# Kernel tuning notes

Measured on AMD Instinct MI355X. Metric: run time of the kernel, lower is better.

Reference implementation:

```python
import jax, jax.numpy as jnp
import numpy as np

K = 5
PAD = K // 2
EPS = 1e-12  # F.normalize eps


def setup_inputs() -> dict:
    key = jax.random.key(0)
    k1, k2, k3 = jax.random.split(key, 3)
    b, c, h, w = 8, 1024, 64, 64
    out_ch = 1024
    feature = jax.random.normal(k1, (b, c, h, w), dtype=jnp.float32)
    # Conv2d(1024 + K*K, out_ch, 1) -> weight [out_ch, 1049], bias [out_ch]
    conv_w = jax.random.normal(k2, (out_ch, c + K * K), dtype=jnp.float32) * 0.02
    conv_b = jax.random.normal(k3, (out_ch,), dtype=jnp.float32) * 0.02
    return {"feature": feature, "conv_w": conv_w, "conv_b": conv_b}


def reference(feature, conv_w, conv_b):
    b, c, h, w = feature.shape
    # L2-normalize over channel dim (F.normalize: x / max(||x||, eps))
    norm = jnp.sqrt(jnp.sum(feature * feature, axis=1, keepdims=True))
    fn = feature / jnp.maximum(norm, EPS)
    fp = jnp.pad(fn, ((0, 0), (0, 0), (PAD, PAD), (PAD, PAD)))
    # 25 shifted correlations; order matches torch loop: index = col*K + row
    corr = jnp.stack(
        [jnp.sum(fp[:, :, r:h + r, cc:w + cc] * fn, axis=1)
         for cc in range(K) for r in range(K)],
        axis=1,
    )  # [b, K*K, h, w]
    cat = jnp.concatenate([feature, corr], axis=1)  # [b, c+K*K, h, w]
    y = jnp.einsum('oc,bchw->bohw', conv_w, cat) + conv_b[None, :, None, None]
    return jax.nn.relu(y)
```

## Files before the change

### kernel.cpp

```cpp
#include <hip/hip_runtime.h>
#include <hip/hip_bf16.h>


typedef __attribute__((ext_vector_type(8))) short short8x;
typedef __attribute__((ext_vector_type(4))) float floatx4;

#define B_   8
#define C_   1024
#define HW_  4096
#define KPAD 1088
#define NT   17

__device__ __forceinline__ unsigned short f2bf(float f) {
  unsigned int u = __float_as_uint(f);
  u += 0x7FFFu + ((u >> 16) & 1u);
  return (unsigned short)(u >> 16);
}
__device__ __forceinline__ float bf2f(unsigned short s) {
  return __uint_as_float(((unsigned int)s) << 16);
}

__device__ __forceinline__ void async16(const void* g, void* l) {
  __builtin_amdgcn_global_load_lds(
      (__attribute__((address_space(1))) void*)(void*)g,
      (__attribute__((address_space(3))) void*)l, 16, 0, 0);
}

__device__ __forceinline__ short8x rd16(const char* p) {
  return *(const short8x*)p;
}

__global__ __launch_bounds__(512) void scn_corr_part(
    const float* __restrict__ f, float* __restrict__ part) {
  const int tid = threadIdx.x;
  const int x = tid & 63;
  const int y = blockIdx.x * 8 + (tid >> 6);
  const int cs = blockIdx.y, b = blockIdx.z;

  const int xs0 = (x + 2 < 64) ? x + 2 : 63;
  const int xs1 = (x + 1 < 64) ? x + 1 : 63;
  const int xs3 = (x - 1 >= 0) ? x - 1 : 0;
  const int xs4 = (x - 2 >= 0) ? x - 2 : 0;

  const bool ym2 = (y >= 2), ym1 = (y >= 1), yp1 = (y <= 62), yp2 = (y <= 61);

  const float* rp0 = f + ((size_t)b * C_ + cs * 128) * HW_ + y * 64;

  float h[25];
#pragma unroll
  for (int j = 0; j < 25; ++j) h[j] = 0.f;

#pragma unroll 4
  for (int c = 0; c < 128; ++c) {
    const float* rp = rp0 + (size_t)c * HW_;
    const float ctr = rp[x];
    const float vm2 = ym2 ? rp[x - 128] : 0.f;
    const float vm1 = ym1 ? rp[x - 64] : 0.f;
    const float vp1 = yp1 ? rp[x + 64] : 0.f;
    const float vp2 = yp2 ? rp[x + 128] : 0.f;
    const float c0 = rp[xs0], c1 = rp[xs1], c3 = rp[xs3], c4 = rp[xs4];
    const float v[5] = {vm2, vm1, ctr, vp1, vp2};
    const float cc[5] = {c0, c1, ctr, c3, c4};
#pragma unroll
    for (int dxi = 0; dxi < 5; ++dxi)
#pragma unroll
      for (int dyi = 0; dyi < 5; ++dyi)
        h[dxi * 5 + dyi] = fmaf(v[dyi], cc[dxi], h[dxi * 5 + dyi]);
  }

  float* pb = part + (size_t)(cs * 25) * 32768 + b * HW_ + y * 64;
#pragma unroll
  for (int j = 0; j < 25; ++j) {
    const int dx = (j / 5) - 2;
    const int tgt = x - dx;
    const int wx = (tgt + 64) & 63;
    const float val = ((unsigned)tgt < 64u) ? h[j] : 0.f;
    pb[(size_t)j * 32768 + wx] = val;
  }
}

__global__ __launch_bounds__(256) void scn_transpose(
    const float* __restrict__ f, unsigned short* __restrict__ At) {
  __shared__ float lds[64][65];
  const int mt = blockIdx.x, kt = blockIdx.y, b = blockIdx.z;
  const int tid = threadIdx.x;
  const float* src = f + ((size_t)b * C_ + kt * 64) * HW_ + mt * 64;
  const int mi = tid & 63, kr = tid >> 6;
#pragma unroll
  for (int i = 0; i < 16; ++i)
    lds[kr + i * 4][mi] = src[(size_t)(kr + i * 4) * HW_ + mi];
  __syncthreads();
  unsigned short* dst = At + ((size_t)b * HW_ + mt * 64) * KPAD + kt * 64;
  const int c = tid & 7, mr = tid >> 3;
#pragma unroll
  for (int half = 0; half < 2; ++half) {
    const int mm = mr + half * 32;
    short8x v;
#pragma unroll
    for (int j = 0; j < 8; ++j) v[j] = (short)f2bf(lds[c * 8 + j][mm]);
    *(short8x*)(dst + (size_t)mm * KPAD + c * 8) = v;
  }
}

__global__ __launch_bounds__(256) void scn_invn(const float* __restrict__ part,
                                                float* __restrict__ invn) {
  const int i = blockIdx.x * 256 + threadIdx.x;
  float s = 0.f;
#pragma unroll
  for (int cs = 0; cs < 8; ++cs) s += part[(size_t)(cs * 25 + 12) * 32768 + i];
  invn[i] = 1.0f / fmaxf(sqrtf(s), 1e-12f);
}

__global__ __launch_bounds__(256) void scn_corr_reduce(
    const float* __restrict__ part, const float* __restrict__ invn,
    unsigned short* __restrict__ At) {
  const int b = blockIdx.y;
  const int m = blockIdx.x * 256 + threadIdx.x;
  const int i = b * HW_ + m;
  const int y = m >> 6, x = m & 63;

  float acc[25];
#pragma unroll
  for (int j = 0; j < 25; ++j) acc[j] = 0.f;
#pragma unroll 1
  for (int cs = 0; cs < 8; ++cs) {
    const float* pb = part + (size_t)(cs * 25) * 32768 + i;
#pragma unroll
    for (int j = 0; j < 25; ++j) acc[j] += pb[(size_t)j * 32768];
  }
  const float ic = invn[i];
  unsigned short r[64];
#pragma unroll
  for (int j = 0; j < 25; ++j) {
    const int dy = (j % 5) - 2, dx = (j / 5) - 2;
    const int ny = y + dy, nx = x + dx;
    float in2 = (ny >= 0 && ny < 64 && nx >= 0 && nx < 64)
                    ? invn[b * HW_ + (ny << 6) + nx] : 0.f;
    r[j] = f2bf(acc[j] * ic * in2);
  }
#pragma unroll
  for (int j = 25; j < 64; ++j) r[j] = 0;
  unsigned short* row = At + ((size_t)b * HW_ + m) * KPAD + 1024;
#pragma unroll
  for (int v = 0; v < 8; ++v) *(short8x*)(row + v * 8) = *(short8x*)(r + v * 8);
}

__global__ __launch_bounds__(256) void scn_wcast(const float* __restrict__ w,
                                                 unsigned short* __restrict__ Wb) {
  const int i = blockIdx.x * 256 + threadIdx.x;
  const int o = i / KPAD, k = i - o * KPAD;
  Wb[i] = (k < 1049) ? f2bf(w[(size_t)o * 1049 + k]) : 0;
}

__global__ __launch_bounds__(512, 2) void scn_gemm(
    const unsigned short* __restrict__ Wb, const unsigned short* __restrict__ At,
    const float* __restrict__ bias, float* __restrict__ out) {
  extern __shared__ char lds[];
  const int tid = threadIdx.x;
  const int l = tid & 63;
  const int wid = tid >> 6;
  const int wm = wid >> 2;
  const int wn = wid & 3;
  const int nb = blockIdx.x, ob = blockIdx.y, b = blockIdx.z;

  const int rr = tid >> 3;
  const int cswz = ((tid & 7) ^ (rr & 7)) << 3;
  const unsigned short* gA = Wb + (size_t)(ob * 256 + rr) * KPAD + cswz;
  const unsigned short* gB = At + ((size_t)b * HW_ + nb * 256 + rr) * KPAD + cswz;
  char* const dBase = (char*)lds + tid * 16;

#define ISSUE_A(bf, kt)                                         \
  do {                                                          \
    const unsigned short* _s = gA + (kt) * 64;                  \
    char* _d = dBase + (bf) * 65536;                            \
    async16(_s, _d);                                            \
    async16(_s + (size_t)64 * KPAD, _d + 8192);                 \
    async16(_s + (size_t)128 * KPAD, _d + 16384);               \
    async16(_s + (size_t)192 * KPAD, _d + 24576);               \
  } while (0)

#define ISSUE_B(bf, kt)                                         \
  do {                                                          \
    const unsigned short* _s = gB + (kt) * 64;                  \
    char* _d = dBase + (bf) * 65536 + 32768;                    \
    async16(_s, _d);                                            \
    async16(_s + (size_t)64 * KPAD, _d + 8192);                 \
    async16(_s + (size_t)128 * KPAD, _d + 16384);               \
    async16(_s + (size_t)192 * KPAD, _d + 24576);               \
  } while (0)

  const int l15 = l & 15, l4g = l >> 4, l7 = l & 7;
  const int aoff0 = l15 * 128 + ((l4g ^ l7) << 4);
  const int aoff1 = l15 * 128 + (((l4g + 4) ^ l7) << 4);
  const char* aB0 = (const char*)lds + wm * 16384;
  const char* bB0 = (const char*)lds + 32768 + (wn >> 1) * 16384 + (wn & 1) * 8192;

  floatx4 acc[8][4];
#pragma unroll
  for (int i = 0; i < 8; ++i)
#pragma unroll
    for (int j = 0; j < 4; ++j) acc[i][j] = (floatx4){0.f, 0.f, 0.f, 0.f};

  ISSUE_A(0, 0); ISSUE_B(0, 0);
  ISSUE_A(1, 1); ISSUE_B(1, 1);
  asm volatile("s_waitcnt vmcnt(8)" ::: "memory");
  __builtin_amdgcn_s_barrier();

  short8x a[4][2], b0[2][2], b1[2][2];

  for (int t = 0; t < NT; ++t) {
    const int bf = t & 1;
    const char* ab = aB0 + bf * 65536;
    const char* bb = bB0 + bf * 65536;
    const int t2 = (t < NT - 2) ? (t + 2) : 0;

#pragma unroll
    for (int i = 0; i < 4; ++i) {
      a[i][0] = rd16(ab + i * 2048 + aoff0);
      a[i][1] = rd16(ab + i * 2048 + aoff1);
    }
#pragma unroll
    for (int j = 0; j < 2; ++j) {
      b0[j][0] = rd16(bb + j * 2048 + aoff0);
      b0[j][1] = rd16(bb + j * 2048 + aoff1);
    }
    __builtin_amdgcn_s_barrier();
    asm volatile("s_waitcnt lgkmcnt(0)" ::: "memory");
    __builtin_amdgcn_sched_barrier(0);
    __builtin_amdgcn_s_setprio(1);
#pragma unroll
    for (int i = 0; i < 4; ++i)
#pragma unroll
      for (int j = 0; j < 2; ++j) {
        acc[i][j] = __builtin_amdgcn_mfma_f32_16x16x32_bf16(a[i][0], b0[j][0], acc[i][j], 0, 0, 0);
        acc[i][j] = __builtin_amdgcn_mfma_f32_16x16x32_bf16(a[i][1], b0[j][1], acc[i][j], 0, 0, 0);
      }
    __builtin_amdgcn_s_setprio(0);
    __builtin_amdgcn_s_barrier();

#pragma unroll
    for (int j = 0; j < 2; ++j) {
      b1[j][0] = rd16(bb + (2 + j) * 2048 + aoff0);
      b1[j][1] = rd16(bb + (2 + j) * 2048 + aoff1);
    }
    __builtin_amdgcn_s_barrier();
    asm volatile("s_waitcnt lgkmcnt(0)" ::: "memory");
    __builtin_amdgcn_sched_barrier(0);
    __builtin_amdgcn_s_setprio(1);
#pragma unroll
    for (int i = 0; i < 4; ++i)
#pragma unroll
      for (int j = 0; j < 2; ++j) {
        acc[i][2 + j] = __builtin_amdgcn_mfma_f32_16x16x32_bf16(a[i][0], b1[j][0], acc[i][2 + j], 0, 0, 0);
        acc[i][2 + j] = __builtin_amdgcn_mfma_f32_16x16x32_bf16(a[i][1], b1[j][1], acc[i][2 + j], 0, 0, 0);
      }
    __builtin_amdgcn_s_setprio(0);
    __builtin_amdgcn_s_barrier();

#pragma unroll
    for (int i = 0; i < 4; ++i) {
      a[i][0] = rd16(ab + (4 + i) * 2048 + aoff0);
      a[i][1] = rd16(ab + (4 + i) * 2048 + aoff1);
    }
    ISSUE_B(bf, t2);
    __builtin_amdgcn_s_barrier();
    asm volatile("s_waitcnt lgkmcnt(0)" ::: "memory");
    __builtin_amdgcn_sched_barrier(0);
    __builtin_amdgcn_s_setprio(1);
#pragma unroll
    for (int i = 0; i < 4; ++i)
#pragma unroll
      for (int j = 0; j < 2; ++j) {
        acc[4 + i][2 + j] = __builtin_amdgcn_mfma_f32_16x16x32_bf16(a[i][0], b1[j][0], acc[4 + i][2 + j], 0, 0, 0);
        acc[4 + i][2 + j] = __builtin_amdgcn_mfma_f32_16x16x32_bf16(a[i][1], b1[j][1], acc[4 + i][2 + j], 0, 0, 0);
      }
    __builtin_amdgcn_s_setprio(0);
    __builtin_amdgcn_s_barrier();

    ISSUE_A(bf, t2);
    __builtin_amdgcn_s_barrier();
    __builtin_amdgcn_s_setprio(1);
#pragma unroll
    for (int i = 0; i < 4; ++i)
#pragma unroll
      for (int j = 0; j < 2; ++j) {
        acc[4 + i][j] = __builtin_amdgcn_mfma_f32_16x16x32_bf16(a[i][0], b0[j][0], acc[4 + i][j], 0, 0, 0);
        acc[4 + i][j] = __builtin_amdgcn_mfma_f32_16x16x32_bf16(a[i][1], b0[j][1], acc[4 + i][j], 0, 0, 0);
      }
    __builtin_amdgcn_s_setprio(0);
    asm volatile("s_waitcnt vmcnt(8)" ::: "memory");
    __builtin_amdgcn_s_barrier();
  }
  asm volatile("s_waitcnt vmcnt(0)" ::: "memory");
#undef ISSUE_A
#undef ISSUE_B

  float* outb = out + (size_t)b * C_ * HW_;
#pragma unroll
  for (int i = 0; i < 8; ++i) {
    const int o0 = ob * 256 + wm * 128 + i * 16 + l4g * 4;
    float bs[4];
#pragma unroll
    for (int r = 0; r < 4; ++r) bs[r] = bias[o0 + r];
#pragma unroll
    for (int j = 0; j < 4; ++j) {
      const int m = nb * 256 + wn * 64 + j * 16 + l15;
#pragma unroll
      for (int r = 0; r < 4; ++r) {
        float v = acc[i][j][r] + bs[r];
        outb[(size_t)(o0 + r) * HW_ + m] = v > 0.f ? v : 0.f;
      }
    }
  }
}

extern "C" void kernel_launch(void* const* d_in, const int* in_sizes, int n_in,
                              void* d_out, int out_size, void* d_ws, size_t ws_size,
                              hipStream_t stream) {
  const float* feature = (const float*)d_in[0];
  const float* conv_w  = (const float*)d_in[1];
  const float* conv_b  = (const float*)d_in[2];
  float* out = (float*)d_out;

  char* ws = (char*)d_ws;
  unsigned short* At = (unsigned short*)(ws);
  float* part        = (float*)(ws + 71303168);
  unsigned short* Wb = (unsigned short*)(ws + 71303168);
  float* invn        = (float*)(ws + 97517568);

  static int gemm_attr_set = 0;
  if (!gemm_attr_set) {
    hipFuncSetAttribute((const void*)scn_gemm,
                        hipFuncAttributeMaxDynamicSharedMemorySize, 131072);
    gemm_attr_set = 1;
  }

  scn_corr_part<<<dim3(8, 8, 8), 512, 0, stream>>>(feature, part);
  scn_transpose<<<dim3(64, 16, 8), 256, 0, stream>>>(feature, At);
  scn_invn<<<dim3(128), 256, 0, stream>>>(part, invn);
  scn_corr_reduce<<<dim3(16, 8), 256, 0, stream>>>(part, invn, At);
  scn_wcast<<<dim3((1024 * KPAD) / 256), 256, 0, stream>>>(conv_w, Wb);
  scn_gemm<<<dim3(16, 4, 8), 512, 131072, stream>>>(Wb, At, conv_b, out);
}
```

Measured before the change: 383.2 us.

## Fuse bf16 transpose of features into correlation partial kernel

The separate transpose kernel, which re-read the whole fp32 feature tensor to build the bf16 K-major GEMM operand, is removed. The correlation kernel now converts each centre value it already loads to bf16, stages a 512x64 tile in LDS, and writes the transposed rows to At after each 64-channel half. This saves one full read of the 128 MB input and one kernel launch. In exchange the correlation kernel gains about 66 KB of LDS, which can lower occupancy, plus two extra barriers per half.

```diff
diff --git a/kernel.cpp b/kernel.cpp
--- a/kernel.cpp
+++ b/kernel.cpp
@@ -16,9 +16,6 @@
   u += 0x7FFFu + ((u >> 16) & 1u);
   return (unsigned short)(u >> 16);
 }
-__device__ __forceinline__ float bf2f(unsigned short s) {
-  return __uint_as_float(((unsigned int)s) << 16);
-}
 
 __device__ __forceinline__ void async16(const void* g, void* l) {
   __builtin_amdgcn_global_load_lds(
@@ -31,7 +28,10 @@
 }
 
 __global__ __launch_bounds__(512) void scn_corr_part(
-    const float* __restrict__ f, float* __restrict__ part) {
+    const float* __restrict__ f, float* __restrict__ part,
+    unsigned short* __restrict__ At) {
+  __shared__ unsigned short lct[512][66];
+
   const int tid = threadIdx.x;
   const int x = tid & 63;
   const int y = blockIdx.x * 8 + (tid >> 6);
@@ -50,22 +50,43 @@
 #pragma unroll
   for (int j = 0; j < 25; ++j) h[j] = 0.f;
 
+  unsigned short* const lrow = &lct[tid][0];
+  const int m0 = blockIdx.x * 512;
+  const int cslice = tid & 7, mbase = tid >> 3;
+
+  for (int half = 0; half < 2; ++half) {
 #pragma unroll 4
-  for (int c = 0; c < 128; ++c) {
-    const float* rp = rp0 + (size_t)c * HW_;
-    const float ctr = rp[x];
-    const float vm2 = ym2 ? rp[x - 128] : 0.f;
-    const float vm1 = ym1 ? rp[x - 64] : 0.f;
-    const float vp1 = yp1 ? rp[x + 64] : 0.f;
-    const float vp2 = yp2 ? rp[x + 128] : 0.f;
-    const float c0 = rp[xs0], c1 = rp[xs1], c3 = rp[xs3], c4 = rp[xs4];
-    const float v[5] = {vm2, vm1, ctr, vp1, vp2};
-    const float cc[5] = {c0, c1, ctr, c3, c4};
-#pragma unroll
-    for (int dxi = 0; dxi < 5; ++dxi)
-#pragma unroll
-      for (int dyi = 0; dyi < 5; ++dyi)
-        h[dxi * 5 + dyi] = fmaf(v[dyi], cc[dxi], h[dxi * 5 + dyi]);
+    for (int c64 = 0; c64 < 64; ++c64) {
+      const int c = half * 64 + c64;
+      const float* rp = rp0 + (size_t)c * HW_;
+      const float ctr = rp[x];
+      const float vm2 = ym2 ? rp[x - 128] : 0.f;
+      const float vm1 = ym1 ? rp[x - 64] : 0.f;
+      const float vp1 = yp1 ? rp[x + 64] : 0.f;
+      const float vp2 = yp2 ? rp[x + 128] : 0.f;
+      const float c0 = rp[xs0], c1 = rp[xs1], c3 = rp[xs3], c4 = rp[xs4];
+      lrow[c64] = f2bf(ctr);
+      const float v[5] = {vm2, vm1, ctr, vp1, vp2};
+      const float cc[5] = {c0, c1, ctr, c3, c4};
+#pragma unroll
+      for (int dxi = 0; dxi < 5; ++dxi)
+#pragma unroll
+        for (int dyi = 0; dyi < 5; ++dyi)
+          h[dxi * 5 + dyi] = fmaf(v[dyi], cc[dxi], h[dxi * 5 + dyi]);
+    }
+    __syncthreads();
+    const int k0 = cs * 128 + half * 64;
+#pragma unroll
+    for (int g = 0; g < 8; ++g) {
+      const int mm = mbase + g * 64;
+      const unsigned int* p =
+          (const unsigned int*)((const char*)&lct[mm][0] + cslice * 16);
+      unsigned int w0 = p[0], w1 = p[1], w2 = p[2], w3 = p[3];
+      unsigned int* dst = (unsigned int*)(At + ((size_t)b * HW_ + m0 + mm) * KPAD +
+                                          k0 + cslice * 8);
+      dst[0] = w0; dst[1] = w1; dst[2] = w2; dst[3] = w3;
+    }
+    __syncthreads();
   }
 
   float* pb = part + (size_t)(cs * 25) * 32768 + b * HW_ + y * 64;
@@ -76,29 +97,6 @@
     const int wx = (tgt + 64) & 63;
     const float val = ((unsigned)tgt < 64u) ? h[j] : 0.f;
     pb[(size_t)j * 32768 + wx] = val;
-  }
-}
-
-__global__ __launch_bounds__(256) void scn_transpose(
-    const float* __restrict__ f, unsigned short* __restrict__ At) {
-  __shared__ float lds[64][65];
-  const int mt = blockIdx.x, kt = blockIdx.y, b = blockIdx.z;
-  const int tid = threadIdx.x;
-  const float* src = f + ((size_t)b * C_ + kt * 64) * HW_ + mt * 64;
-  const int mi = tid & 63, kr = tid >> 6;
-#pragma unroll
-  for (int i = 0; i < 16; ++i)
-    lds[kr + i * 4][mi] = src[(size_t)(kr + i * 4) * HW_ + mi];
-  __syncthreads();
-  unsigned short* dst = At + ((size_t)b * HW_ + mt * 64) * KPAD + kt * 64;
-  const int c = tid & 7, mr = tid >> 3;
-#pragma unroll
-  for (int half = 0; half < 2; ++half) {
-    const int mm = mr + half * 32;
-    short8x v;
-#pragma unroll
-    for (int j = 0; j < 8; ++j) v[j] = (short)f2bf(lds[c * 8 + j][mm]);
-    *(short8x*)(dst + (size_t)mm * KPAD + c * 8) = v;
   }
 }
 
@@ -335,8 +333,7 @@
     gemm_attr_set = 1;
   }
 
-  scn_corr_part<<<dim3(8, 8, 8), 512, 0, stream>>>(feature, part);
-  scn_transpose<<<dim3(64, 16, 8), 256, 0, stream>>>(feature, At);
+  scn_corr_part<<<dim3(8, 8, 8), 512, 0, stream>>>(feature, part, At);
   scn_invn<<<dim3(128), 256, 0, stream>>>(part, invn);
   scn_corr_reduce<<<dim3(16, 8), 256, 0, stream>>>(part, invn, At);
   scn_wcast<<<dim3((1024 * KPAD) / 256), 256, 0, stream>>>(conv_w, Wb);
```

Measured after the change: 460.3 us. 1.2x slower.

## Fuse correlation-partial and transpose kernels into one interleaved launch, use shuffles

Applied to the files above, without the earlier changes.

Merges the shifted-correlation partial-sum kernel and the bf16 transpose kernel into a single launch of 4608 blocks. Every ninth block runs correlation work and the other eight each transpose two 64x64 tiles, so the long-running correlation blocks overlap with memory-bound transposes and one launch is removed. Horizontal neighbor loads in the correlation loop are replaced with wave shuffles of the center value. The cost is that correlation blocks now reserve the larger LDS footprint they never use, which can lower occupancy for them.

```diff
diff --git a/kernel.cpp b/kernel.cpp
--- a/kernel.cpp
+++ b/kernel.cpp
@@ -16,9 +16,6 @@
   u += 0x7FFFu + ((u >> 16) & 1u);
   return (unsigned short)(u >> 16);
 }
-__device__ __forceinline__ float bf2f(unsigned short s) {
-  return __uint_as_float(((unsigned int)s) << 16);
-}
 
 __device__ __forceinline__ void async16(const void* g, void* l) {
   __builtin_amdgcn_global_load_lds(
@@ -30,75 +27,84 @@
   return *(const short8x*)p;
 }
 
-__global__ __launch_bounds__(512) void scn_corr_part(
-    const float* __restrict__ f, float* __restrict__ part) {
+__global__ __launch_bounds__(512) void scn_aux(
+    const float* __restrict__ f, float* __restrict__ part,
+    unsigned short* __restrict__ At) {
+  __shared__ float lds2[2][64][65];
+  const int n = blockIdx.x;
+  const int g = n / 9, r = n - g * 9;
   const int tid = threadIdx.x;
-  const int x = tid & 63;
-  const int y = blockIdx.x * 8 + (tid >> 6);
-  const int cs = blockIdx.y, b = blockIdx.z;
-
-  const int xs0 = (x + 2 < 64) ? x + 2 : 63;
-  const int xs1 = (x + 1 < 64) ? x + 1 : 63;
-  const int xs3 = (x - 1 >= 0) ? x - 1 : 0;
-  const int xs4 = (x - 2 >= 0) ? x - 2 : 0;
-
-  const bool ym2 = (y >= 2), ym1 = (y >= 1), yp1 = (y <= 62), yp2 = (y <= 61);
-
-  const float* rp0 = f + ((size_t)b * C_ + cs * 128) * HW_ + y * 64;
-
-  float h[25];
-#pragma unroll
-  for (int j = 0; j < 25; ++j) h[j] = 0.f;
+
+  if (r == 0) {
+    const int x = tid & 63;
+    const int y = (g & 7) * 8 + (tid >> 6);
+    const int cs = (g >> 3) & 7, b = g >> 6;
+
+    const int xs0 = (x + 2 < 64) ? x + 2 : 63;
+    const int xs1 = (x + 1 < 64) ? x + 1 : 63;
+    const int xs3 = (x - 1 >= 0) ? x - 1 : 0;
+    const int xs4 = (x - 2 >= 0) ? x - 2 : 0;
+
+    const bool ym2 = (y >= 2), ym1 = (y >= 1), yp1 = (y <= 62), yp2 = (y <= 61);
+
+    const float* rp0 = f + ((size_t)b * C_ + cs * 128) * HW_ + y * 64;
+
+    float h[25];
+#pragma unroll
+    for (int j = 0; j < 25; ++j) h[j] = 0.f;
 
 #pragma unroll 4
-  for (int c = 0; c < 128; ++c) {
-    const float* rp = rp0 + (size_t)c * HW_;
-    const float ctr = rp[x];
-    const float vm2 = ym2 ? rp[x - 128] : 0.f;
-    const float vm1 = ym1 ? rp[x - 64] : 0.f;
-    const float vp1 = yp1 ? rp[x + 64] : 0.f;
-    const float vp2 = yp2 ? rp[x + 128] : 0.f;
-    const float c0 = rp[xs0], c1 = rp[xs1], c3 = rp[xs3], c4 = rp[xs4];
-    const float v[5] = {vm2, vm1, ctr, vp1, vp2};
-    const float cc[5] = {c0, c1, ctr, c3, c4};
-#pragma unroll
-    for (int dxi = 0; dxi < 5; ++dxi)
-#pragma unroll
-      for (int dyi = 0; dyi < 5; ++dyi)
-        h[dxi * 5 + dyi] = fmaf(v[dyi], cc[dxi], h[dxi * 5 + dyi]);
-  }
-
-  float* pb = part + (size_t)(cs * 25) * 32768 + b * HW_ + y * 64;
-#pragma unroll
-  for (int j = 0; j < 25; ++j) {
-    const int dx = (j / 5) - 2;
-    const int tgt = x - dx;
-    const int wx = (tgt + 64) & 63;
-    const float val = ((unsigned)tgt < 64u) ? h[j] : 0.f;
-    pb[(size_t)j * 32768 + wx] = val;
-  }
-}
-
-__global__ __launch_bounds__(256) void scn_transpose(
-    const float* __restrict__ f, unsigned short* __restrict__ At) {
-  __shared__ float lds[64][65];
-  const int mt = blockIdx.x, kt = blockIdx.y, b = blockIdx.z;
-  const int tid = threadIdx.x;
-  const float* src = f + ((size_t)b * C_ + kt * 64) * HW_ + mt * 64;
-  const int mi = tid & 63, kr = tid >> 6;
-#pragma unroll
-  for (int i = 0; i < 16; ++i)
-    lds[kr + i * 4][mi] = src[(size_t)(kr + i * 4) * HW_ + mi];
-  __syncthreads();
-  unsigned short* dst = At + ((size_t)b * HW_ + mt * 64) * KPAD + kt * 64;
-  const int c = tid & 7, mr = tid >> 3;
-#pragma unroll
-  for (int half = 0; half < 2; ++half) {
-    const int mm = mr + half * 32;
-    short8x v;
-#pragma unroll
-    for (int j = 0; j < 8; ++j) v[j] = (short)f2bf(lds[c * 8 + j][mm]);
-    *(short8x*)(dst + (size_t)mm * KPAD + c * 8) = v;
+    for (int c = 0; c < 128; ++c) {
+      const float* rp = rp0 + (size_t)c * HW_;
+      const float ctr = rp[x];
+      const float vm2 = ym2 ? rp[x - 128] : 0.f;
+      const float vm1 = ym1 ? rp[x - 64] : 0.f;
+      const float vp1 = yp1 ? rp[x + 64] : 0.f;
+      const float vp2 = yp2 ? rp[x + 128] : 0.f;
+      const float c0 = __shfl(ctr, xs0, 64);
+      const float c1 = __shfl(ctr, xs1, 64);
+      const float c3 = __shfl(ctr, xs3, 64);
+      const float c4 = __shfl(ctr, xs4, 64);
+      const float v[5] = {vm2, vm1, ctr, vp1, vp2};
+      const float cc[5] = {c0, c1, ctr, c3, c4};
+#pragma unroll
+      for (int dxi = 0; dxi < 5; ++dxi)
+#pragma unroll
+        for (int dyi = 0; dyi < 5; ++dyi)
+          h[dxi * 5 + dyi] = fmaf(v[dyi], cc[dxi], h[dxi * 5 + dyi]);
+    }
+
+    float* pb = part + (size_t)(cs * 25) * 32768 + b * HW_ + y * 64;
+#pragma unroll
+    for (int j = 0; j < 25; ++j) {
+      const int dx = (j / 5) - 2;
+      const int tgt = x - dx;
+      const int wx = (tgt + 64) & 63;
+      const float val = ((unsigned)tgt < 64u) ? h[j] : 0.f;
+      pb[(size_t)j * 32768 + wx] = val;
+    }
+  } else {
+    const int half = tid >> 8, t256 = tid & 255;
+    const int tile = (g * 8 + (r - 1)) * 2 + half;
+    const int b = tile >> 10, rem = tile & 1023;
+    const int kt = rem >> 6, mt = rem & 63;
+
+    const float* src = f + ((size_t)b * C_ + kt * 64) * HW_ + mt * 64;
+    const int mi = t256 & 63, kr = t256 >> 6;
+#pragma unroll
+    for (int i = 0; i < 16; ++i)
+      lds2[half][kr + i * 4][mi] = src[(size_t)(kr + i * 4) * HW_ + mi];
+    __syncthreads();
+    unsigned short* dst = At + ((size_t)b * HW_ + mt * 64) * KPAD + kt * 64;
+    const int c = t256 & 7, mr = t256 >> 3;
+#pragma unroll
+    for (int h2 = 0; h2 < 2; ++h2) {
+      const int mm = mr + h2 * 32;
+      short8x v;
+#pragma unroll
+      for (int j = 0; j < 8; ++j) v[j] = (short)f2bf(lds2[half][c * 8 + j][mm]);
+      *(short8x*)(dst + (size_t)mm * KPAD + c * 8) = v;
+    }
   }
 }
 
@@ -335,8 +341,7 @@
     gemm_attr_set = 1;
   }
 
-  scn_corr_part<<<dim3(8, 8, 8), 512, 0, stream>>>(feature, part);
-  scn_transpose<<<dim3(64, 16, 8), 256, 0, stream>>>(feature, At);
+  scn_aux<<<dim3(4608), 512, 0, stream>>>(feature, part, At);
   scn_invn<<<dim3(128), 256, 0, stream>>>(part, invn);
   scn_corr_reduce<<<dim3(16, 8), 256, 0, stream>>>(part, invn, At);
   scn_wcast<<<dim3((1024 * KPAD) / 256), 256, 0, stream>>>(conv_w, Wb);
```

Measured after the change: 388.3 us. No clear change (+1.3%).
